# Performance work log

Measured on AMD Instinct MI355X. Metric: run time of the kernel, lower is better.

## Reference

```python
import jax, jax.numpy as jnp
import numpy as np
from jax import lax

NQ = 12   # num_qubits
NL = 6    # num_layers
NC = 64   # num_classes
BATCH = 512
TWO_PI = 6.283185307179586


def _bcast(v):
    # broadcast a per-batch scalar (B,) against state (B, 2,...,2)
    return v.reshape((-1,) + (1,) * NQ) if v.ndim == 1 else v


def _apply_rx(state, theta, wire):
    """Apply RX(theta) on `wire`. state: (B,)+(2,)*NQ complex64.
    RX(t) = [[cos(t/2), -i sin(t/2)], [-i sin(t/2), cos(t/2)]]."""
    c = _bcast(jnp.cos(theta / 2))
    s = _bcast(jnp.sin(theta / 2))
    ax = 1 + wire  # wire 0 is the most significant qubit (PennyLane ordering)
    s0 = lax.index_in_dim(state, 0, ax, keepdims=True)
    s1 = lax.index_in_dim(state, 1, ax, keepdims=True)
    n0 = c * s0 - 1j * s * s1
    n1 = -1j * s * s0 + c * s1
    return jnp.concatenate([n0, n1], axis=ax)


def _apply_cnot(state, ctrl, tgt):
    ac, at = 1 + ctrl, 1 + tgt
    s0 = lax.index_in_dim(state, 0, ac, keepdims=True)
    s1 = lax.index_in_dim(state, 1, ac, keepdims=True)
    s1 = jnp.flip(s1, axis=at)  # X on target where control = 1
    return jnp.concatenate([s0, s1], axis=ac)


def _circuit(x, qweights):
    """AngleEmbedding (RX) + BasicEntanglerLayers (RX + ring CNOTs) -> <Z_i>."""
    B = x.shape[0]
    state = jnp.zeros((B,) + (2,) * NQ, jnp.complex64)
    state = state.at[(slice(None),) + (0,) * NQ].set(1.0)  # |0...0>
    # AngleEmbedding: RX(x[:, w]) on wire w (per-sample angles)
    for w in range(NQ):
        state = _apply_rx(state, x[:, w], w)
    # BasicEntanglerLayers: per layer RX rotations then ring of CNOTs
    for l in range(NL):
        for w in range(NQ):
            state = _apply_rx(state, qweights[l, w], w)
        for w in range(NQ):
            state = _apply_cnot(state, w, (w + 1) % NQ)
    probs = jnp.real(state) ** 2 + jnp.imag(state) ** 2  # (B, 2,...,2) float32
    zs = []
    for w in range(NQ):
        other = tuple(a for a in range(1, NQ + 1) if a != 1 + w)
        marg = probs.sum(axis=other)  # (B, 2)
        zs.append(marg[:, 0] - marg[:, 1])  # <Z_w>
    return jnp.stack(zs, axis=1)  # (B, NQ)


def setup_inputs() -> dict:
    key = jax.random.key(0)
    k1, k2, k3 = jax.random.split(key, 3)
    x = jax.random.normal(k1, (BATCH, NQ), dtype=jnp.float32)
    qweights = jax.random.uniform(k2, (NL, NQ), dtype=jnp.float32) * TWO_PI
    W = jax.random.normal(k3, (NC, NQ), dtype=jnp.float32) * 0.1
    b = jnp.zeros((NC,), dtype=jnp.float32)
    return {"x": x, "qweights": qweights, "W": W, "b": b}


def reference(x, qweights, W, b):
    z = _circuit(x, qweights)          # (B, NQ) expectation values
    return z @ W.T + b                  # (B, NC) classifier logits
```

## Files before the change

### kernel.cpp

```cpp
#include <hip/hip_runtime.h>

#define NQB   12
#define NST   4096
#define NLAY  6
#define NCLS  64
#define NGQ   72
#define TPB   512

struct PhiArgs  { int m[NGQ]; };
struct MainArgs { int meas[NQB]; };

__global__ __launch_bounds__(64) void phiq_kernel(
    const float* __restrict__ qw, float* __restrict__ phiq, PhiArgs A)
{
    const int k = blockIdx.x * 64 + threadIdx.x;
    float acc = 0.f;
    #pragma unroll
    for (int g = 0; g < NGQ; ++g) {
        float v = 0.5f * qw[g];
        acc += (__popc(k & A.m[g]) & 1) ? -v : v;
    }
    phiq[k] = acc;
}

__global__ __launch_bounds__(TPB) void qnn_kernel(
    const float* __restrict__ x, const float* __restrict__ phiq,
    const float* __restrict__ W, const float* __restrict__ bias,
    float* __restrict__ out, MainArgs A)
{
    __shared__ float2 d[NST];
    __shared__ float  zpart[TPB / 64][NQB];
    __shared__ float  zfin[NQB];

    const int tid = threadIdx.x;
    const int b   = blockIdx.x;

    float pq[8];
    #pragma unroll
    for (int r = 0; r < 8; ++r) pq[r] = phiq[tid + (r << 9)];

    float xv[NQB];
    #pragma unroll
    for (int w = 0; w < NQB; ++w) xv[w] = 0.5f * x[b * NQB + w];
    float base = 0.f;
    #pragma unroll
    for (int w = 3; w < NQB; ++w)
        base += ((tid >> (11 - w)) & 1) ? -xv[w] : xv[w];
    float c3[8];
    #pragma unroll
    for (int r = 0; r < 8; ++r)
        c3[r] = ((r & 4) ? -xv[0] : xv[0]) + ((r & 2) ? -xv[1] : xv[1])
              + ((r & 1) ? -xv[2] : xv[2]);

    float2 myd[8];
    #pragma unroll
    for (int r = 0; r < 8; ++r) {
        float phi = pq[r] + base + c3[r];
        float rv = phi * 0.15915494309189535f;
        rv -= floorf(rv);
        float sv = __builtin_amdgcn_sinf(rv);
        float cv = __builtin_amdgcn_cosf(rv);
        myd[r] = make_float2(cv, sv);
        d[tid + (r << 9)] = myd[r];
    }
    __syncthreads();

    float acc[NQB];
    #pragma unroll
    for (int w = 0; w < NQB; ++w) acc[w] = 0.f;
    #pragma unroll
    for (int w = 0; w < NQB; ++w) {
        const int u = tid ^ A.meas[w];
        #pragma unroll
        for (int r = 0; r < 8; ++r) {
            float2 p = d[u ^ (r << 9)];
            acc[w] = fmaf(myd[r].x, p.x, fmaf(myd[r].y, p.y, acc[w]));
        }
    }

    const int lane = tid & 63, wid = tid >> 6;
    #pragma unroll
    for (int w = 0; w < NQB; ++w) {
        float v = acc[w];
        #pragma unroll
        for (int off = 32; off > 0; off >>= 1) v += __shfl_down(v, off);
        if (lane == 0) zpart[wid][w] = v;
    }
    __syncthreads();
    if (tid < NQB) {
        float v = 0.f;
        #pragma unroll
        for (int k = 0; k < TPB / 64; ++k) v += zpart[k][tid];
        zfin[tid] = v * (1.0f / NST);
    }
    __syncthreads();

    if (tid < NCLS) {
        float a = bias[tid];
        #pragma unroll
        for (int w = 0; w < NQB; ++w) a += zfin[w] * W[tid * NQB + w];
        out[b * NCLS + tid] = a;
    }
}


static int f_of(int j) {
    for (int w = 11; w >= 0; --w) {
        int pc = 11 - w;
        int pt = 11 - ((w + 1) % 12);
        j ^= ((j >> pc) & 1) << pt;
    }
    return j;
}

static void build_args(PhiArgs* P, MainArgs* M) {
    for (int l = 0; l < NLAY; ++l)
        for (int w = 0; w < NQB; ++w) {
            int v = 1 << (11 - w);
            for (int t = 0; t < l; ++t) v = f_of(v);
            P->m[l * NQB + w] = v;
        }
    int col[NQB];
    for (int k = 0; k < NQB; ++k) {
        int v = 1 << k;
        for (int t = 0; t < NLAY; ++t) v = f_of(v);
        col[k] = v;
    }
    unsigned rowG[NQB], rowH[NQB];
    for (int r = 0; r < NQB; ++r) {
        unsigned rr = 0;
        for (int k = 0; k < NQB; ++k) rr |= ((unsigned)((col[k] >> r) & 1)) << k;
        rowG[r] = rr;
        rowH[r] = 1u << r;
    }
    for (int k = 0; k < NQB; ++k) {
        int piv = -1;
        for (int r = k; r < NQB; ++r)
            if ((rowG[r] >> k) & 1) { piv = r; break; }
        unsigned tg = rowG[piv], th = rowH[piv];
        rowG[piv] = rowG[k]; rowH[piv] = rowH[k];
        rowG[k] = tg; rowH[k] = th;
        for (int r = 0; r < NQB; ++r)
            if (r != k && ((rowG[r] >> k) & 1)) { rowG[r] ^= rowG[k]; rowH[r] ^= rowH[k]; }
    }
    for (int w = 0; w < NQB; ++w) M->meas[w] = (int)rowH[11 - w];
}

extern "C" void kernel_launch(void* const* d_in, const int* in_sizes, int n_in,
                              void* d_out, int out_size, void* d_ws, size_t ws_size,
                              hipStream_t stream) {
    const float* x    = (const float*)d_in[0];
    const float* qw   = (const float*)d_in[1];
    const float* W    = (const float*)d_in[2];
    const float* bias = (const float*)d_in[3];
    float* out        = (float*)d_out;
    float* phiq       = (float*)d_ws;

    PhiArgs P; MainArgs M;
    build_args(&P, &M);

    const int batch = in_sizes[0] / NQB;
    phiq_kernel<<<64, 64, 0, stream>>>(qw, phiq, P);
    qnn_kernel<<<batch, TPB, 0, stream>>>(x, phiq, W, bias, out, M);
}
```

Measured before the change: 72.54 us.

## Permute qubit bit order to halve symmetric LDS reads in the Z-expectation loop

```diff
diff --git a/kernel.cpp b/kernel.cpp
--- a/kernel.cpp
+++ b/kernel.cpp
@@ -8,7 +8,13 @@
 #define TPB   512
 
 struct PhiArgs  { int m[NGQ]; };
-struct MainArgs { int meas[NQB]; };
+struct MainArgs {
+    int   wire_of_bit[NQB];
+    int   mlo[NQB];
+    int   h[NQB];
+    int   rmask[NQB];
+    float wgt[NQB];
+};
 
 __global__ __launch_bounds__(64) void phiq_kernel(
     const float* __restrict__ qw, float* __restrict__ phiq, PhiArgs A)
@@ -39,18 +45,20 @@
     #pragma unroll
     for (int r = 0; r < 8; ++r) pq[r] = phiq[tid + (r << 9)];
 
-    float xv[NQB];
-    #pragma unroll
-    for (int w = 0; w < NQB; ++w) xv[w] = 0.5f * x[b * NQB + w];
+    float xl[NQB];
+    #pragma unroll
+    for (int p = 0; p < NQB; ++p)
+        xl[p] = 0.5f * x[b * NQB + A.wire_of_bit[p]];
     float base = 0.f;
     #pragma unroll
-    for (int w = 3; w < NQB; ++w)
-        base += ((tid >> (11 - w)) & 1) ? -xv[w] : xv[w];
+    for (int p = 0; p < 9; ++p)
+        base += ((tid >> p) & 1) ? -xl[p] : xl[p];
     float c3[8];
     #pragma unroll
     for (int r = 0; r < 8; ++r)
-        c3[r] = ((r & 4) ? -xv[0] : xv[0]) + ((r & 2) ? -xv[1] : xv[1])
-              + ((r & 1) ? -xv[2] : xv[2]);
+        c3[r] = ((r & 1) ? -xl[9]  : xl[9])
+              + ((r & 2) ? -xl[10] : xl[10])
+              + ((r & 4) ? -xl[11] : xl[11]);
 
     float2 myd[8];
     #pragma unroll
@@ -67,15 +75,18 @@
 
     float acc[NQB];
     #pragma unroll
-    for (int w = 0; w < NQB; ++w) acc[w] = 0.f;
-    #pragma unroll
     for (int w = 0; w < NQB; ++w) {
-        const int u = tid ^ A.meas[w];
+        const int u  = tid ^ A.mlo[w];
+        const int hw = A.h[w];
+        float aw = 0.f;
         #pragma unroll
         for (int r = 0; r < 8; ++r) {
-            float2 p = d[u ^ (r << 9)];
-            acc[w] = fmaf(myd[r].x, p.x, fmaf(myd[r].y, p.y, acc[w]));
+            if (A.rmask[w] & (1 << r)) {
+                float2 p = d[u | ((hw ^ r) << 9)];
+                aw = fmaf(myd[r].x, p.x, fmaf(myd[r].y, p.y, aw));
+            }
         }
+        acc[w] = aw * A.wgt[w];
     }
 
     const int lane = tid & 63, wid = tid >> 6;
@@ -91,7 +102,7 @@
         float v = 0.f;
         #pragma unroll
         for (int k = 0; k < TPB / 64; ++k) v += zpart[k][tid];
-        zfin[tid] = v * (1.0f / NST);
+        zfin[tid] = v;
     }
     __syncthreads();
 
@@ -114,11 +125,12 @@
 }
 
 static void build_args(PhiArgs* P, MainArgs* M) {
+    int lm[NGQ];
     for (int l = 0; l < NLAY; ++l)
         for (int w = 0; w < NQB; ++w) {
             int v = 1 << (11 - w);
             for (int t = 0; t < l; ++t) v = f_of(v);
-            P->m[l * NQB + w] = v;
+            lm[l * NQB + w] = v;
         }
     int col[NQB];
     for (int k = 0; k < NQB; ++k) {
@@ -143,7 +155,44 @@
         for (int r = 0; r < NQB; ++r)
             if (r != k && ((rowG[r] >> k) & 1)) { rowG[r] ^= rowG[k]; rowH[r] ^= rowH[k]; }
     }
-    for (int w = 0; w < NQB; ++w) M->meas[w] = (int)rowH[11 - w];
+    int meas_nat[NQB];
+    for (int w = 0; w < NQB; ++w) meas_nat[w] = (int)rowH[11 - w];
+
+    int bc0 = 0, bc1 = 1, bc2 = 2, best = -1;
+    for (int a = 0; a < NQB; ++a)
+        for (int bb = a + 1; bb < NQB; ++bb)
+            for (int c = bb + 1; c < NQB; ++c) {
+                int sel = (1 << a) | (1 << bb) | (1 << c), cov = 0;
+                for (int w = 0; w < NQB; ++w) if (meas_nat[w] & sel) ++cov;
+                if (cov > best) { best = cov; bc0 = a; bc1 = bb; bc2 = c; }
+            }
+    int sigma[NQB];
+    sigma[bc0] = 9; sigma[bc1] = 10; sigma[bc2] = 11;
+    int nxt = 0;
+    for (int j = 0; j < NQB; ++j)
+        if (j != bc0 && j != bc1 && j != bc2) sigma[j] = nxt++;
+    auto pm = [&](int m) {
+        int o = 0;
+        for (int j = 0; j < NQB; ++j) if ((m >> j) & 1) o |= 1 << sigma[j];
+        return o;
+    };
+
+    for (int g = 0; g < NGQ; ++g) P->m[g] = pm(lm[g]);
+    for (int w = 0; w < NQB; ++w) M->wire_of_bit[sigma[11 - w]] = w;
+
+    for (int w = 0; w < NQB; ++w) {
+        int t = pm(meas_nat[w]);
+        M->mlo[w] = t & 511;
+        M->h[w]   = t >> 9;
+        if (M->h[w]) {
+            int bsel = __builtin_ctz(M->h[w]);
+            M->rmask[w] = (bsel == 0) ? 0x55 : (bsel == 1) ? 0x33 : 0x0F;
+            M->wgt[w]   = 2.0f / NST;
+        } else {
+            M->rmask[w] = 0xFF;
+            M->wgt[w]   = 1.0f / NST;
+        }
+    }
 }
 
 extern "C" void kernel_launch(void* const* d_in, const int* in_sizes, int n_in,
```

Result: faster. 70.10 us (-3.4%).

## Change state basis so measurement masks become single-bit flips; register-local reductions

Applied to the files above, without the earlier changes.

```diff
diff --git a/kernel.cpp b/kernel.cpp
--- a/kernel.cpp
+++ b/kernel.cpp
@@ -6,9 +6,14 @@
 #define NCLS  64
 #define NGQ   72
 #define TPB   512
+#define RS    10
+#define ZST   516
 
 struct PhiArgs  { int m[NGQ]; };
-struct MainArgs { int meas[NQB]; };
+struct MainArgs {
+    int emlo[NQB];
+    int ehi[NQB];
+};
 
 __global__ __launch_bounds__(64) void phiq_kernel(
     const float* __restrict__ qw, float* __restrict__ phiq, PhiArgs A)
@@ -28,8 +33,9 @@
     const float* __restrict__ W, const float* __restrict__ bias,
     float* __restrict__ out, MainArgs A)
 {
-    __shared__ float2 d[NST];
-    __shared__ float  zpart[TPB / 64][NQB];
+    __shared__ float2 dd[TPB * RS];
+    __shared__ float  zmat[NQB * ZST];
+    __shared__ float  part2[NQB * 32];
     __shared__ float  zfin[NQB];
 
     const int tid = threadIdx.x;
@@ -39,59 +45,82 @@
     #pragma unroll
     for (int r = 0; r < 8; ++r) pq[r] = phiq[tid + (r << 9)];
 
-    float xv[NQB];
-    #pragma unroll
-    for (int w = 0; w < NQB; ++w) xv[w] = 0.5f * x[b * NQB + w];
-    float base = 0.f;
-    #pragma unroll
-    for (int w = 3; w < NQB; ++w)
-        base += ((tid >> (11 - w)) & 1) ? -xv[w] : xv[w];
-    float c3[8];
-    #pragma unroll
-    for (int r = 0; r < 8; ++r)
-        c3[r] = ((r & 4) ? -xv[0] : xv[0]) + ((r & 2) ? -xv[1] : xv[1])
-              + ((r & 1) ? -xv[2] : xv[2]);
+    float px[8];
+    #pragma unroll
+    for (int r = 0; r < 8; ++r) px[r] = 0.f;
+    #pragma unroll
+    for (int w = 0; w < NQB; ++w) {
+        float xv = 0.5f * x[b * NQB + w];
+        float sv = (__popc(tid & A.emlo[w]) & 1) ? -xv : xv;
+        const int hi = A.ehi[w];
+        #pragma unroll
+        for (int r = 0; r < 8; ++r)
+            px[r] += (__popc(r & hi) & 1) ? -sv : sv;
+    }
 
     float2 myd[8];
     #pragma unroll
     for (int r = 0; r < 8; ++r) {
-        float phi = pq[r] + base + c3[r];
+        float phi = pq[r] + px[r];
         float rv = phi * 0.15915494309189535f;
         rv -= floorf(rv);
-        float sv = __builtin_amdgcn_sinf(rv);
-        float cv = __builtin_amdgcn_cosf(rv);
-        myd[r] = make_float2(cv, sv);
-        d[tid + (r << 9)] = myd[r];
+        myd[r] = make_float2(__builtin_amdgcn_cosf(rv),
+                             __builtin_amdgcn_sinf(rv));
+    }
+    {
+        float4* wr = (float4*)&dd[tid * RS];
+        #pragma unroll
+        for (int h = 0; h < 4; ++h)
+            wr[h] = make_float4(myd[2 * h].x, myd[2 * h].y,
+                                myd[2 * h + 1].x, myd[2 * h + 1].y);
     }
     __syncthreads();
 
     float acc[NQB];
     #pragma unroll
-    for (int w = 0; w < NQB; ++w) acc[w] = 0.f;
-    #pragma unroll
-    for (int w = 0; w < NQB; ++w) {
-        const int u = tid ^ A.meas[w];
-        #pragma unroll
-        for (int r = 0; r < 8; ++r) {
-            float2 p = d[u ^ (r << 9)];
-            acc[w] = fmaf(myd[r].x, p.x, fmaf(myd[r].y, p.y, acc[w]));
+    for (int p = 0; p < 9; ++p) {
+        float aw = 0.f;
+        if (!((tid >> p) & 1)) {
+            const float4* row = (const float4*)&dd[(tid ^ (1 << p)) * RS];
+            #pragma unroll
+            for (int h = 0; h < 4; ++h) {
+                float4 q = row[h];
+                aw = fmaf(myd[2 * h].x, q.x, fmaf(myd[2 * h].y, q.y, aw));
+                aw = fmaf(myd[2 * h + 1].x, q.z,
+                          fmaf(myd[2 * h + 1].y, q.w, aw));
+            }
         }
-    }
-
-    const int lane = tid & 63, wid = tid >> 6;
-    #pragma unroll
-    for (int w = 0; w < NQB; ++w) {
-        float v = acc[w];
-        #pragma unroll
-        for (int off = 32; off > 0; off >>= 1) v += __shfl_down(v, off);
-        if (lane == 0) zpart[wid][w] = v;
+        acc[p] = aw;
+    }
+    {
+        auto dot2 = [&](int i, int j) {
+            return fmaf(myd[i].x, myd[j].x, myd[i].y * myd[j].y);
+        };
+        acc[9]  = dot2(0,1) + dot2(2,3) + dot2(4,5) + dot2(6,7);
+        acc[10] = dot2(0,2) + dot2(1,3) + dot2(4,6) + dot2(5,7);
+        acc[11] = dot2(0,4) + dot2(1,5) + dot2(2,6) + dot2(3,7);
+    }
+
+    #pragma unroll
+    for (int w = 0; w < NQB; ++w) zmat[w * ZST + tid] = acc[w];
+    __syncthreads();
+    if (tid < NQB * 32) {
+        const int w = tid >> 5, seg = tid & 31;
+        const float4* rowz = (const float4*)&zmat[w * ZST];
+        float s = 0.f;
+        #pragma unroll
+        for (int i = 0; i < 4; ++i) {
+            float4 q = rowz[seg * 4 + i];
+            s += (q.x + q.y) + (q.z + q.w);
+        }
+        part2[w * 32 + seg] = s;
     }
     __syncthreads();
     if (tid < NQB) {
-        float v = 0.f;
-        #pragma unroll
-        for (int k = 0; k < TPB / 64; ++k) v += zpart[k][tid];
-        zfin[tid] = v * (1.0f / NST);
+        float s = 0.f;
+        #pragma unroll
+        for (int i = 0; i < 32; ++i) s += part2[tid * 32 + i];
+        zfin[tid] = s * (2.0f / NST);
     }
     __syncthreads();
 
@@ -114,11 +143,12 @@
 }
 
 static void build_args(PhiArgs* P, MainArgs* M) {
+    int lm[NGQ];
     for (int l = 0; l < NLAY; ++l)
         for (int w = 0; w < NQB; ++w) {
             int v = 1 << (11 - w);
             for (int t = 0; t < l; ++t) v = f_of(v);
-            P->m[l * NQB + w] = v;
+            lm[l * NQB + w] = v;
         }
     int col[NQB];
     for (int k = 0; k < NQB; ++k) {
@@ -143,7 +173,23 @@
         for (int r = 0; r < NQB; ++r)
             if (r != k && ((rowG[r] >> k) & 1)) { rowG[r] ^= rowG[k]; rowH[r] ^= rowH[k]; }
     }
-    for (int w = 0; w < NQB; ++w) M->meas[w] = (int)rowH[11 - w];
+    int meas_nat[NQB];
+    for (int w = 0; w < NQB; ++w) meas_nat[w] = (int)rowH[11 - w];
+
+    int Tm[NQB];
+    for (int w = 0; w < NQB; ++w) Tm[w] = meas_nat[w];
+    auto xf = [&](int m) {
+        int o = 0;
+        for (int bb = 0; bb < NQB; ++bb)
+            if (__builtin_popcount((unsigned)(Tm[bb] & m)) & 1) o |= 1 << bb;
+        return o;
+    };
+    for (int g = 0; g < NGQ; ++g) P->m[g] = xf(lm[g]);
+    for (int w = 0; w < NQB; ++w) {
+        int e = xf(1 << (11 - w));
+        M->emlo[w] = e & 511;
+        M->ehi[w]  = e >> 9;
+    }
 }
 
 extern "C" void kernel_launch(void* const* d_in, const int* in_sizes, int n_in,
```

After: 66.08 us. 8.9% less time.
